# Kernel optimization log

Hardware: AMD Instinct MI355X
Metric: run time of the kernel (lower is better)

The kernel has to match this reference:

```python
import jax, jax.numpy as jnp
import numpy as np

B = 131072
USER_N = 100000
ITEM_N = 20000
CONCEPT_N = 128
D_IN = 3
NB_MOD_MAX = 12
M = NB_MOD_MAX + 2  # nb_mod_max_plus_sent


def setup_inputs() -> dict:
    key = jax.random.key(0)
    ks = jax.random.split(key, 7)
    user_ids = jax.random.randint(ks[0], (B,), 0, USER_N)
    item_ids = jax.random.randint(ks[1], (B,), 0, ITEM_N)
    concept_ids = jax.random.randint(ks[2], (B,), 0, CONCEPT_N)
    users_emb_weight = jax.random.normal(ks[3], (USER_N, CONCEPT_N), dtype=jnp.float32)
    item_resp_weight = jax.random.normal(ks[4], (ITEM_N * M, D_IN), dtype=jnp.float32)
    W = jax.random.normal(ks[5], (CONCEPT_N, D_IN, CONCEPT_N), dtype=jnp.float32)
    # nb_modalities in [2, nb_mod_max]; mask[i, j] = 0 for j in [1, nb_modalities[i]], inf elsewhere
    nb_modalities = jax.random.randint(ks[6], (ITEM_N,), 2, NB_MOD_MAX + 1)
    cols = jnp.arange(M)[None, :]  # (1, M)
    valid = (cols >= 1) & (cols <= nb_modalities[:, None])
    mask = jnp.where(valid, 0.0, jnp.inf).astype(jnp.float32)  # (ITEM_N, M)
    return {
        "user_ids": user_ids,
        "item_ids": item_ids,
        "concept_ids": concept_ids,
        "users_emb_weight": users_emb_weight,
        "item_resp_weight": item_resp_weight,
        "W": W,
        "mask": mask,
        "nb_modalities": nb_modalities,
    }


def reference(user_ids, item_ids, concept_ids, users_emb_weight, item_resp_weight, W, mask, nb_modalities):
    # W_t: (B, d_in, C)
    W_t = W[concept_ids]
    # im_idx: (B, M) row indices into the item-response embedding table
    im_idx = item_ids[:, None] * M + jnp.arange(M)[None, :]
    im_emb_prime = item_resp_weight[im_idx]  # (B, M, d_in)
    # bmm: (B, M, d_in) x (B, d_in, C) -> (B, M, C)
    im_emb = jnp.einsum('bmd,bdc->bmc', im_emb_prime, W_t)
    u_emb = users_emb_weight[user_ids]  # (B, C)
    diff = u_emb[:, None, :] - im_emb
    p_uim = jnp.sum(diff * diff, axis=2)  # (B, M)
    idx = jnp.argmin(p_uim + mask[item_ids, :], axis=1)  # (B,)
    nb = nb_modalities[item_ids]
    # mod_to_resp: ((idx - 1) / (nb - 1)) + 1
    responses = (idx.astype(jnp.float32) - 1.0) / (nb.astype(jnp.float32) - 1.0) + 1.0
    return responses
```

## Files before the change

kernel.cpp:

```cpp
#include <hip/hip_runtime.h>
#include <math.h>

static constexpr int B_TOTAL   = 131072;
static constexpr int M_MOD     = 14;
static constexpr int C_DIM     = 128;
static constexpr int CONCEPT_N = 128;

__global__ __launch_bounds__(64) void gram_kernel(
    const float* __restrict__ W,
    float*       __restrict__ Gt)
{
    const int c = blockIdx.x;
    const int l = threadIdx.x;
    const float* wp = W + (size_t)c * 3 * C_DIM;
    float g00 = 0.f, g01 = 0.f, g02 = 0.f, g11 = 0.f, g12 = 0.f, g22 = 0.f;
#pragma unroll
    for (int k = 0; k < 2; ++k) {
        const int col = l + 64 * k;
        const float a0 = wp[col];
        const float a1 = wp[C_DIM + col];
        const float a2 = wp[2 * C_DIM + col];
        g00 = fmaf(a0, a0, g00); g01 = fmaf(a0, a1, g01);
        g02 = fmaf(a0, a2, g02); g11 = fmaf(a1, a1, g11);
        g12 = fmaf(a1, a2, g12); g22 = fmaf(a2, a2, g22);
    }
#pragma unroll
    for (int off = 32; off; off >>= 1) {
        g00 += __shfl_xor(g00, off, 64);
        g01 += __shfl_xor(g01, off, 64);
        g02 += __shfl_xor(g02, off, 64);
        g11 += __shfl_xor(g11, off, 64);
        g12 += __shfl_xor(g12, off, 64);
        g22 += __shfl_xor(g22, off, 64);
    }
    if (l == 0) {
        float* gp = Gt + (size_t)c * 8;
        gp[0] = g00; gp[1] = g01; gp[2] = g02; gp[3] = g11;
        gp[4] = g12; gp[5] = g22; gp[6] = 0.f; gp[7] = 0.f;
    }
}

template <bool PRECOMP_G>
__global__ __launch_bounds__(256) void impact_kernel(
    const int*   __restrict__ user_ids,
    const int*   __restrict__ item_ids,
    const int*   __restrict__ concept_ids,
    const float* __restrict__ users_emb,
    const float* __restrict__ item_resp,
    const float* __restrict__ W,
    const int*   __restrict__ nb_mod,
    const float* __restrict__ Gt,
    float*       __restrict__ out)
{
    const int s = threadIdx.x & 15;
    const int b = blockIdx.x * 16 + (threadIdx.x >> 4);

    const int uid = user_ids[b];
    const int iid = item_ids[b];
    const int cid = concept_ids[b];
    const int nb  = nb_mod[iid];

    const int jl = (s < 12) ? (s + 1) : 1;
    const float* pj = item_resp + ((size_t)iid * M_MOD + jl) * 3;
    const float p0 = pj[0], p1 = pj[1], p2 = pj[2];

    const float4* up = (const float4*)(users_emb + (size_t)uid * C_DIM);
    const float4 uA = up[s], uB = up[s + 16];
    const float4* wp = (const float4*)(W + (size_t)cid * 3 * C_DIM);
    const float4 w0a = wp[s],      w0b = wp[16 + s];
    const float4 w1a = wp[32 + s], w1b = wp[48 + s];
    const float4 w2a = wp[64 + s], w2b = wp[80 + s];

    float v0 = 0.f, v1 = 0.f, v2 = 0.f;
    float g00, g01, g02, g11, g12, g22;

    if (PRECOMP_G) {
        const float4* gp = (const float4*)(Gt + (size_t)cid * 8);
        const float4 gA = gp[0], gB = gp[1];
        g00 = gA.x; g01 = gA.y; g02 = gA.z; g11 = gA.w;
        g12 = gB.x; g22 = gB.y;
#define COLV(uc, a0, a1, a2)                                                   \
        do {                                                                   \
            v0 = fmaf((a0), (uc), v0);                                         \
            v1 = fmaf((a1), (uc), v1);                                         \
            v2 = fmaf((a2), (uc), v2);                                         \
        } while (0)
        COLV(uA.x, w0a.x, w1a.x, w2a.x);
        COLV(uA.y, w0a.y, w1a.y, w2a.y);
        COLV(uA.z, w0a.z, w1a.z, w2a.z);
        COLV(uA.w, w0a.w, w1a.w, w2a.w);
        COLV(uB.x, w0b.x, w1b.x, w2b.x);
        COLV(uB.y, w0b.y, w1b.y, w2b.y);
        COLV(uB.z, w0b.z, w1b.z, w2b.z);
        COLV(uB.w, w0b.w, w1b.w, w2b.w);
#undef COLV
#pragma unroll
        for (int off = 8; off; off >>= 1) {
            v0 += __shfl_xor(v0, off, 64);
            v1 += __shfl_xor(v1, off, 64);
            v2 += __shfl_xor(v2, off, 64);
        }
    } else {
        g00 = 0.f; g01 = 0.f; g02 = 0.f; g11 = 0.f; g12 = 0.f; g22 = 0.f;
#define COL(uc, a0, a1, a2)                                                    \
        do {                                                                   \
            v0  = fmaf((a0), (uc), v0);  v1  = fmaf((a1), (uc), v1);           \
            v2  = fmaf((a2), (uc), v2);                                        \
            g00 = fmaf((a0), (a0), g00); g01 = fmaf((a0), (a1), g01);          \
            g02 = fmaf((a0), (a2), g02); g11 = fmaf((a1), (a1), g11);          \
            g12 = fmaf((a1), (a2), g12); g22 = fmaf((a2), (a2), g22);          \
        } while (0)
        COL(uA.x, w0a.x, w1a.x, w2a.x);
        COL(uA.y, w0a.y, w1a.y, w2a.y);
        COL(uA.z, w0a.z, w1a.z, w2a.z);
        COL(uA.w, w0a.w, w1a.w, w2a.w);
        COL(uB.x, w0b.x, w1b.x, w2b.x);
        COL(uB.y, w0b.y, w1b.y, w2b.y);
        COL(uB.z, w0b.z, w1b.z, w2b.z);
        COL(uB.w, w0b.w, w1b.w, w2b.w);
#undef COL
#pragma unroll
        for (int off = 8; off; off >>= 1) {
            v0  += __shfl_xor(v0,  off, 64);
            v1  += __shfl_xor(v1,  off, 64);
            v2  += __shfl_xor(v2,  off, 64);
            g00 += __shfl_xor(g00, off, 64);
            g01 += __shfl_xor(g01, off, 64);
            g02 += __shfl_xor(g02, off, 64);
            g11 += __shfl_xor(g11, off, 64);
            g12 += __shfl_xor(g12, off, 64);
            g22 += __shfl_xor(g22, off, 64);
        }
    }

    float m = INFINITY;
    if (s < 12 && (s + 1) <= nb) {
        const float dot = fmaf(p0, v0, fmaf(p1, v1, p2 * v2));
        float q = p0 * p0 * g00;
        q = fmaf(p1 * p1, g11, q);
        q = fmaf(p2 * p2, g22, q);
        q = fmaf(2.0f * p0 * p1, g01, q);
        q = fmaf(2.0f * p0 * p2, g02, q);
        q = fmaf(2.0f * p1 * p2, g12, q);
        m = fmaf(-2.0f, dot, q);
    }
    float bm = m;
#pragma unroll
    for (int off = 8; off; off >>= 1)
        bm = fminf(bm, __shfl_xor(bm, off, 64));
    const unsigned long long mask = __ballot(m == bm);
    if (s == 0) {
        const int group = (threadIdx.x >> 4) & 3;
        const unsigned slice = (unsigned)((mask >> (group * 16)) & 0xffffu);
        const int jm1 = __builtin_ctz(slice);
        out[b] = (float)jm1 / (float)(nb - 1) + 1.0f;
    }
}

extern "C" void kernel_launch(void* const* d_in, const int* in_sizes, int n_in,
                              void* d_out, int out_size, void* d_ws, size_t ws_size,
                              hipStream_t stream) {
    const int*   user_ids    = (const int*)d_in[0];
    const int*   item_ids    = (const int*)d_in[1];
    const int*   concept_ids = (const int*)d_in[2];
    const float* users_emb   = (const float*)d_in[3];
    const float* item_resp   = (const float*)d_in[4];
    const float* W           = (const float*)d_in[5];
    const int*   nb_mod      = (const int*)d_in[7];
    float*       out         = (float*)d_out;

    const size_t gram_bytes = (size_t)CONCEPT_N * 8 * sizeof(float);

    dim3 grid(B_TOTAL / 16), block(256);
    if (d_ws != nullptr && ws_size >= gram_bytes) {
        float* Gt = (float*)d_ws;
        gram_kernel<<<dim3(CONCEPT_N), dim3(64), 0, stream>>>(W, Gt);
        impact_kernel<true><<<grid, block, 0, stream>>>(
            user_ids, item_ids, concept_ids, users_emb, item_resp, W, nb_mod,
            Gt, out);
    } else {
        impact_kernel<false><<<grid, block, 0, stream>>>(
            user_ids, item_ids, concept_ids, users_emb, item_resp, W, nb_mod,
            nullptr, out);
    }
}
```

Measured before the change: 113.7 us.

## Drop Gram precompute kernel and process two batch rows per 16-lane group

Removes the separate Gram-matrix kernel and computes the 3x3 Gram terms inline in the main kernel, so only one kernel is launched. Each 16-lane group now handles two batch rows, with all gathers for both rows issued up front to raise memory-level parallelism. The grid is halved and launch bounds request 4 blocks per CU. The cost is extra per-row FMAs and shuffles for the Gram terms plus higher register pressure from holding two rows of W and user embeddings.

```diff
diff --git a/kernel.cpp b/kernel.cpp
--- a/kernel.cpp
+++ b/kernel.cpp
@@ -1,47 +1,11 @@
 #include <hip/hip_runtime.h>
 #include <math.h>
 
-static constexpr int B_TOTAL   = 131072;
-static constexpr int M_MOD     = 14;
-static constexpr int C_DIM     = 128;
-static constexpr int CONCEPT_N = 128;
+static constexpr int B_TOTAL = 131072;
+static constexpr int M_MOD   = 14;
+static constexpr int C_DIM   = 128;
 
-__global__ __launch_bounds__(64) void gram_kernel(
-    const float* __restrict__ W,
-    float*       __restrict__ Gt)
-{
-    const int c = blockIdx.x;
-    const int l = threadIdx.x;
-    const float* wp = W + (size_t)c * 3 * C_DIM;
-    float g00 = 0.f, g01 = 0.f, g02 = 0.f, g11 = 0.f, g12 = 0.f, g22 = 0.f;
-#pragma unroll
-    for (int k = 0; k < 2; ++k) {
-        const int col = l + 64 * k;
-        const float a0 = wp[col];
-        const float a1 = wp[C_DIM + col];
-        const float a2 = wp[2 * C_DIM + col];
-        g00 = fmaf(a0, a0, g00); g01 = fmaf(a0, a1, g01);
-        g02 = fmaf(a0, a2, g02); g11 = fmaf(a1, a1, g11);
-        g12 = fmaf(a1, a2, g12); g22 = fmaf(a2, a2, g22);
-    }
-#pragma unroll
-    for (int off = 32; off; off >>= 1) {
-        g00 += __shfl_xor(g00, off, 64);
-        g01 += __shfl_xor(g01, off, 64);
-        g02 += __shfl_xor(g02, off, 64);
-        g11 += __shfl_xor(g11, off, 64);
-        g12 += __shfl_xor(g12, off, 64);
-        g22 += __shfl_xor(g22, off, 64);
-    }
-    if (l == 0) {
-        float* gp = Gt + (size_t)c * 8;
-        gp[0] = g00; gp[1] = g01; gp[2] = g02; gp[3] = g11;
-        gp[4] = g12; gp[5] = g22; gp[6] = 0.f; gp[7] = 0.f;
-    }
-}
-
-template <bool PRECOMP_G>
-__global__ __launch_bounds__(256) void impact_kernel(
+__global__ __launch_bounds__(256, 4) void impact_kernel(
     const int*   __restrict__ user_ids,
     const int*   __restrict__ item_ids,
     const int*   __restrict__ concept_ids,
@@ -49,112 +13,120 @@
     const float* __restrict__ item_resp,
     const float* __restrict__ W,
     const int*   __restrict__ nb_mod,
-    const float* __restrict__ Gt,
     float*       __restrict__ out)
 {
     const int s = threadIdx.x & 15;
-    const int b = blockIdx.x * 16 + (threadIdx.x >> 4);
+    const int g = threadIdx.x >> 4;
+    const int b0 = blockIdx.x * 32 + g * 2;
+    const int b1 = b0 + 1;
 
-    const int uid = user_ids[b];
-    const int iid = item_ids[b];
-    const int cid = concept_ids[b];
-    const int nb  = nb_mod[iid];
+    const int uid0 = user_ids[b0],    uid1 = user_ids[b1];
+    const int iid0 = item_ids[b0],    iid1 = item_ids[b1];
+    const int cid0 = concept_ids[b0], cid1 = concept_ids[b1];
+    const int nb0  = nb_mod[iid0],    nb1  = nb_mod[iid1];
 
     const int jl = (s < 12) ? (s + 1) : 1;
-    const float* pj = item_resp + ((size_t)iid * M_MOD + jl) * 3;
-    const float p0 = pj[0], p1 = pj[1], p2 = pj[2];
+    const float* pj0 = item_resp + ((size_t)iid0 * M_MOD + jl) * 3;
+    const float* pj1 = item_resp + ((size_t)iid1 * M_MOD + jl) * 3;
+    const float p00 = pj0[0], p01 = pj0[1], p02 = pj0[2];
+    const float p10 = pj1[0], p11 = pj1[1], p12 = pj1[2];
 
-    const float4* up = (const float4*)(users_emb + (size_t)uid * C_DIM);
-    const float4 uA = up[s], uB = up[s + 16];
-    const float4* wp = (const float4*)(W + (size_t)cid * 3 * C_DIM);
-    const float4 w0a = wp[s],      w0b = wp[16 + s];
-    const float4 w1a = wp[32 + s], w1b = wp[48 + s];
-    const float4 w2a = wp[64 + s], w2b = wp[80 + s];
+    const float4* up0 = (const float4*)(users_emb + (size_t)uid0 * C_DIM);
+    const float4* up1 = (const float4*)(users_emb + (size_t)uid1 * C_DIM);
+    const float4 u0A = up0[s], u0B = up0[s + 16];
+    const float4 u1A = up1[s], u1B = up1[s + 16];
 
-    float v0 = 0.f, v1 = 0.f, v2 = 0.f;
-    float g00, g01, g02, g11, g12, g22;
+    const float4* wp0 = (const float4*)(W + (size_t)cid0 * 3 * C_DIM);
+    const float4* wp1 = (const float4*)(W + (size_t)cid1 * 3 * C_DIM);
+    const float4 x0a = wp0[s],      x0b = wp0[16 + s];
+    const float4 x1a = wp0[32 + s], x1b = wp0[48 + s];
+    const float4 x2a = wp0[64 + s], x2b = wp0[80 + s];
+    const float4 y0a = wp1[s],      y0b = wp1[16 + s];
+    const float4 y1a = wp1[32 + s], y1b = wp1[48 + s];
+    const float4 y2a = wp1[64 + s], y2b = wp1[80 + s];
 
-    if (PRECOMP_G) {
-        const float4* gp = (const float4*)(Gt + (size_t)cid * 8);
-        const float4 gA = gp[0], gB = gp[1];
-        g00 = gA.x; g01 = gA.y; g02 = gA.z; g11 = gA.w;
-        g12 = gB.x; g22 = gB.y;
-#define COLV(uc, a0, a1, a2)                                                   \
-        do {                                                                   \
-            v0 = fmaf((a0), (uc), v0);                                         \
-            v1 = fmaf((a1), (uc), v1);                                         \
-            v2 = fmaf((a2), (uc), v2);                                         \
-        } while (0)
-        COLV(uA.x, w0a.x, w1a.x, w2a.x);
-        COLV(uA.y, w0a.y, w1a.y, w2a.y);
-        COLV(uA.z, w0a.z, w1a.z, w2a.z);
-        COLV(uA.w, w0a.w, w1a.w, w2a.w);
-        COLV(uB.x, w0b.x, w1b.x, w2b.x);
-        COLV(uB.y, w0b.y, w1b.y, w2b.y);
-        COLV(uB.z, w0b.z, w1b.z, w2b.z);
-        COLV(uB.w, w0b.w, w1b.w, w2b.w);
-#undef COLV
-#pragma unroll
-        for (int off = 8; off; off >>= 1) {
-            v0 += __shfl_xor(v0, off, 64);
-            v1 += __shfl_xor(v1, off, 64);
-            v2 += __shfl_xor(v2, off, 64);
-        }
-    } else {
-        g00 = 0.f; g01 = 0.f; g02 = 0.f; g11 = 0.f; g12 = 0.f; g22 = 0.f;
 #define COL(uc, a0, a1, a2)                                                    \
-        do {                                                                   \
-            v0  = fmaf((a0), (uc), v0);  v1  = fmaf((a1), (uc), v1);           \
-            v2  = fmaf((a2), (uc), v2);                                        \
-            g00 = fmaf((a0), (a0), g00); g01 = fmaf((a0), (a1), g01);          \
-            g02 = fmaf((a0), (a2), g02); g11 = fmaf((a1), (a1), g11);          \
-            g12 = fmaf((a1), (a2), g12); g22 = fmaf((a2), (a2), g22);          \
-        } while (0)
-        COL(uA.x, w0a.x, w1a.x, w2a.x);
-        COL(uA.y, w0a.y, w1a.y, w2a.y);
-        COL(uA.z, w0a.z, w1a.z, w2a.z);
-        COL(uA.w, w0a.w, w1a.w, w2a.w);
-        COL(uB.x, w0b.x, w1b.x, w2b.x);
-        COL(uB.y, w0b.y, w1b.y, w2b.y);
-        COL(uB.z, w0b.z, w1b.z, w2b.z);
-        COL(uB.w, w0b.w, w1b.w, w2b.w);
-#undef COL
-#pragma unroll
-        for (int off = 8; off; off >>= 1) {
-            v0  += __shfl_xor(v0,  off, 64);
-            v1  += __shfl_xor(v1,  off, 64);
-            v2  += __shfl_xor(v2,  off, 64);
-            g00 += __shfl_xor(g00, off, 64);
-            g01 += __shfl_xor(g01, off, 64);
-            g02 += __shfl_xor(g02, off, 64);
-            g11 += __shfl_xor(g11, off, 64);
-            g12 += __shfl_xor(g12, off, 64);
-            g22 += __shfl_xor(g22, off, 64);
-        }
+    do {                                                                       \
+        v0  = fmaf((a0), (uc), v0);  v1  = fmaf((a1), (uc), v1);               \
+        v2  = fmaf((a2), (uc), v2);                                            \
+        g00 = fmaf((a0), (a0), g00); g01 = fmaf((a0), (a1), g01);              \
+        g02 = fmaf((a0), (a2), g02); g11 = fmaf((a1), (a1), g11);              \
+        g12 = fmaf((a1), (a2), g12); g22 = fmaf((a2), (a2), g22);              \
+    } while (0)
+
+#define REDUCE9()                                                              \
+    _Pragma("unroll")                                                          \
+    for (int off = 8; off; off >>= 1) {                                        \
+        v0  += __shfl_xor(v0,  off, 64);                                       \
+        v1  += __shfl_xor(v1,  off, 64);                                       \
+        v2  += __shfl_xor(v2,  off, 64);                                       \
+        g00 += __shfl_xor(g00, off, 64);                                       \
+        g01 += __shfl_xor(g01, off, 64);                                       \
+        g02 += __shfl_xor(g02, off, 64);                                       \
+        g11 += __shfl_xor(g11, off, 64);                                       \
+        g12 += __shfl_xor(g12, off, 64);                                       \
+        g22 += __shfl_xor(g22, off, 64);                                       \
     }
 
-    float m = INFINITY;
-    if (s < 12 && (s + 1) <= nb) {
-        const float dot = fmaf(p0, v0, fmaf(p1, v1, p2 * v2));
-        float q = p0 * p0 * g00;
-        q = fmaf(p1 * p1, g11, q);
-        q = fmaf(p2 * p2, g22, q);
-        q = fmaf(2.0f * p0 * p1, g01, q);
-        q = fmaf(2.0f * p0 * p2, g02, q);
-        q = fmaf(2.0f * p1 * p2, g12, q);
-        m = fmaf(-2.0f, dot, q);
+#define SCORE_AND_WRITE(P0, P1, P2, NB, BIDX)                                  \
+    do {                                                                       \
+        float m = INFINITY;                                                    \
+        if (s < 12 && (s + 1) <= (NB)) {                                       \
+            const float dot = fmaf((P0), v0, fmaf((P1), v1, (P2) * v2));       \
+            float q = (P0) * (P0) * g00;                                       \
+            q = fmaf((P1) * (P1), g11, q);                                     \
+            q = fmaf((P2) * (P2), g22, q);                                     \
+            q = fmaf(2.0f * (P0) * (P1), g01, q);                              \
+            q = fmaf(2.0f * (P0) * (P2), g02, q);                              \
+            q = fmaf(2.0f * (P1) * (P2), g12, q);                              \
+            m = fmaf(-2.0f, dot, q);                                           \
+        }                                                                      \
+        float bm = m;                                                          \
+        _Pragma("unroll")                                                      \
+        for (int off = 8; off; off >>= 1)                                      \
+            bm = fminf(bm, __shfl_xor(bm, off, 64));                           \
+        const unsigned long long mask = __ballot(m == bm);                     \
+        if (s == 0) {                                                          \
+            const int grp = g & 3;                                             \
+            const unsigned slice = (unsigned)((mask >> (grp * 16)) & 0xffffu); \
+            const int jm1 = __builtin_ctz(slice);                              \
+            out[BIDX] = (float)jm1 / (float)((NB) - 1) + 1.0f;                 \
+        }                                                                      \
+    } while (0)
+
+    {
+        float v0 = 0.f, v1 = 0.f, v2 = 0.f;
+        float g00 = 0.f, g01 = 0.f, g02 = 0.f, g11 = 0.f, g12 = 0.f, g22 = 0.f;
+        COL(u0A.x, x0a.x, x1a.x, x2a.x);
+        COL(u0A.y, x0a.y, x1a.y, x2a.y);
+        COL(u0A.z, x0a.z, x1a.z, x2a.z);
+        COL(u0A.w, x0a.w, x1a.w, x2a.w);
+        COL(u0B.x, x0b.x, x1b.x, x2b.x);
+        COL(u0B.y, x0b.y, x1b.y, x2b.y);
+        COL(u0B.z, x0b.z, x1b.z, x2b.z);
+        COL(u0B.w, x0b.w, x1b.w, x2b.w);
+        REDUCE9();
+        SCORE_AND_WRITE(p00, p01, p02, nb0, b0);
     }
-    float bm = m;
-#pragma unroll
-    for (int off = 8; off; off >>= 1)
-        bm = fminf(bm, __shfl_xor(bm, off, 64));
-    const unsigned long long mask = __ballot(m == bm);
-    if (s == 0) {
-        const int group = (threadIdx.x >> 4) & 3;
-        const unsigned slice = (unsigned)((mask >> (group * 16)) & 0xffffu);
-        const int jm1 = __builtin_ctz(slice);
-        out[b] = (float)jm1 / (float)(nb - 1) + 1.0f;
+
+    {
+        float v0 = 0.f, v1 = 0.f, v2 = 0.f;
+        float g00 = 0.f, g01 = 0.f, g02 = 0.f, g11 = 0.f, g12 = 0.f, g22 = 0.f;
+        COL(u1A.x, y0a.x, y1a.x, y2a.x);
+        COL(u1A.y, y0a.y, y1a.y, y2a.y);
+        COL(u1A.z, y0a.z, y1a.z, y2a.z);
+        COL(u1A.w, y0a.w, y1a.w, y2a.w);
+        COL(u1B.x, y0b.x, y1b.x, y2b.x);
+        COL(u1B.y, y0b.y, y1b.y, y2b.y);
+        COL(u1B.z, y0b.z, y1b.z, y2b.z);
+        COL(u1B.w, y0b.w, y1b.w, y2b.w);
+        REDUCE9();
+        SCORE_AND_WRITE(p10, p11, p12, nb1, b1);
     }
+
+#undef COL
+#undef REDUCE9
+#undef SCORE_AND_WRITE
 }
 
 extern "C" void kernel_launch(void* const* d_in, const int* in_sizes, int n_in,
@@ -169,18 +141,7 @@
     const int*   nb_mod      = (const int*)d_in[7];
     float*       out         = (float*)d_out;
 
-    const size_t gram_bytes = (size_t)CONCEPT_N * 8 * sizeof(float);
-
-    dim3 grid(B_TOTAL / 16), block(256);
-    if (d_ws != nullptr && ws_size >= gram_bytes) {
-        float* Gt = (float*)d_ws;
-        gram_kernel<<<dim3(CONCEPT_N), dim3(64), 0, stream>>>(W, Gt);
-        impact_kernel<true><<<grid, block, 0, stream>>>(
-            user_ids, item_ids, concept_ids, users_emb, item_resp, W, nb_mod,
-            Gt, out);
-    } else {
-        impact_kernel<false><<<grid, block, 0, stream>>>(
-            user_ids, item_ids, concept_ids, users_emb, item_resp, W, nb_mod,
-            nullptr, out);
-    }
+    dim3 grid(B_TOTAL / 32), block(256);
+    impact_kernel<<<grid, block, 0, stream>>>(user_ids, item_ids, concept_ids,
+                                              users_emb, item_resp, W, nb_mod, out);
 }
```

New measurement: 113.1 us. No clear change (-0.6%).

## Bin batch elements by user id to improve embedding gather locality

Applied to the files above, without the earlier changes.

Adds a zero kernel and an atomic scatter kernel that bucket batch indices into 1024 bins by user-id range, then processes elements bin by bin so nearby user embedding rows are read together. The precomputed per-concept Gram matrix is dropped and recomputed inline. This adds two extra launches, atomics, a workspace round trip and many early-exit blocks in exchange for better cache locality on the user table.

```diff
diff --git a/kernel.cpp b/kernel.cpp
--- a/kernel.cpp
+++ b/kernel.cpp
@@ -1,136 +1,124 @@
 #include <hip/hip_runtime.h>
 #include <math.h>
-
-static constexpr int B_TOTAL   = 131072;
-static constexpr int M_MOD     = 14;
-static constexpr int C_DIM     = 128;
-static constexpr int CONCEPT_N = 128;
-
-__global__ __launch_bounds__(64) void gram_kernel(
-    const float* __restrict__ W,
-    float*       __restrict__ Gt)
+#include <stdint.h>
+
+static constexpr int B_TOTAL = 131072;
+static constexpr int M_MOD   = 14;
+static constexpr int C_DIM   = 128;
+
+static constexpr int NBINS    = 1024;
+static constexpr int BIN_CAP  = 256;
+static constexpr int NSLOTS   = NBINS * BIN_CAP;
+static constexpr int BIN_BLKS = NSLOTS / 16;
+static constexpr int OVF_BLKS = B_TOTAL / 16;
+
+static constexpr size_t WS_SLOTS_OFF = 8192;
+static constexpr size_t WS_OVF_OFF   = WS_SLOTS_OFF + (size_t)NSLOTS * 8;
+static constexpr size_t WS_NEEDED    = WS_OVF_OFF + (size_t)B_TOTAL * 8;
+
+__global__ __launch_bounds__(1024) void zero_kernel(uint32_t* __restrict__ cnt) {
+    const int i = threadIdx.x;
+    cnt[i] = 0u;
+    if (i == 0) cnt[NBINS] = 0u;
+}
+
+__global__ __launch_bounds__(256) void scatter_kernel(
+    const int* __restrict__ user_ids,
+    uint32_t*  __restrict__ cnt,
+    uint64_t*  __restrict__ slots,
+    uint64_t*  __restrict__ ovf)
 {
-    const int c = blockIdx.x;
-    const int l = threadIdx.x;
-    const float* wp = W + (size_t)c * 3 * C_DIM;
+    const int e   = blockIdx.x * 256 + threadIdx.x;
+    const int uid = user_ids[e];
+    const int bin = uid >> 7;
+    const uint64_t pk = ((uint64_t)(uint32_t)uid << 32) | (uint32_t)e;
+    const uint32_t r = atomicAdd(&cnt[bin], 1u);
+    if (r < (uint32_t)BIN_CAP) {
+        slots[(size_t)bin * BIN_CAP + r] = pk;
+    } else {
+        const uint32_t o = atomicAdd(&cnt[NBINS], 1u);
+        ovf[o] = pk;
+    }
+}
+
+__global__ __launch_bounds__(256) void impact_binned(
+    const int*      __restrict__ item_ids,
+    const int*      __restrict__ concept_ids,
+    const float*    __restrict__ users_emb,
+    const float*    __restrict__ item_resp,
+    const float*    __restrict__ W,
+    const int*      __restrict__ nb_mod,
+    const uint32_t* __restrict__ cnt,
+    const uint64_t* __restrict__ slots,
+    const uint64_t* __restrict__ ovf,
+    float*          __restrict__ out)
+{
+    const int s = threadIdx.x & 15;
+    const int g = threadIdx.x >> 4;
+
+    uint64_t pk;
+    if (blockIdx.x < BIN_BLKS) {
+        const int bin  = blockIdx.x >> 4;
+        const int base = (blockIdx.x & 15) * 16;
+        uint32_t n = cnt[bin];
+        if (n > (uint32_t)BIN_CAP) n = BIN_CAP;
+        if ((uint32_t)(base + g) >= n) return;
+        pk = slots[(size_t)bin * BIN_CAP + base + g];
+    } else {
+        const uint32_t base = (uint32_t)(blockIdx.x - BIN_BLKS) * 16u;
+        const uint32_t n = cnt[NBINS];
+        if (base + (uint32_t)g >= n) return;
+        pk = ovf[base + g];
+    }
+
+    const int e   = (int)(uint32_t)pk;
+    const int uid = (int)(uint32_t)(pk >> 32);
+    const int iid = item_ids[e];
+    const int cid = concept_ids[e];
+    const int nb  = nb_mod[iid];
+
+    const int jl = (s < 12) ? (s + 1) : 1;
+    const float* pj = item_resp + ((size_t)iid * M_MOD + jl) * 3;
+    const float p0 = pj[0], p1 = pj[1], p2 = pj[2];
+
+    const float4* up = (const float4*)(users_emb + (size_t)uid * C_DIM);
+    const float4 uA = up[s], uB = up[s + 16];
+    const float4* wp = (const float4*)(W + (size_t)cid * 3 * C_DIM);
+    const float4 w0a = wp[s],      w0b = wp[16 + s];
+    const float4 w1a = wp[32 + s], w1b = wp[48 + s];
+    const float4 w2a = wp[64 + s], w2b = wp[80 + s];
+
+    float v0 = 0.f, v1 = 0.f, v2 = 0.f;
     float g00 = 0.f, g01 = 0.f, g02 = 0.f, g11 = 0.f, g12 = 0.f, g22 = 0.f;
-#pragma unroll
-    for (int k = 0; k < 2; ++k) {
-        const int col = l + 64 * k;
-        const float a0 = wp[col];
-        const float a1 = wp[C_DIM + col];
-        const float a2 = wp[2 * C_DIM + col];
-        g00 = fmaf(a0, a0, g00); g01 = fmaf(a0, a1, g01);
-        g02 = fmaf(a0, a2, g02); g11 = fmaf(a1, a1, g11);
-        g12 = fmaf(a1, a2, g12); g22 = fmaf(a2, a2, g22);
-    }
-#pragma unroll
-    for (int off = 32; off; off >>= 1) {
+#define COL(uc, a0, a1, a2)                                                    \
+    do {                                                                       \
+        v0  = fmaf((a0), (uc), v0);  v1  = fmaf((a1), (uc), v1);               \
+        v2  = fmaf((a2), (uc), v2);                                            \
+        g00 = fmaf((a0), (a0), g00); g01 = fmaf((a0), (a1), g01);              \
+        g02 = fmaf((a0), (a2), g02); g11 = fmaf((a1), (a1), g11);              \
+        g12 = fmaf((a1), (a2), g12); g22 = fmaf((a2), (a2), g22);              \
+    } while (0)
+    COL(uA.x, w0a.x, w1a.x, w2a.x);
+    COL(uA.y, w0a.y, w1a.y, w2a.y);
+    COL(uA.z, w0a.z, w1a.z, w2a.z);
+    COL(uA.w, w0a.w, w1a.w, w2a.w);
+    COL(uB.x, w0b.x, w1b.x, w2b.x);
+    COL(uB.y, w0b.y, w1b.y, w2b.y);
+    COL(uB.z, w0b.z, w1b.z, w2b.z);
+    COL(uB.w, w0b.w, w1b.w, w2b.w);
+#undef COL
+
+#pragma unroll
+    for (int off = 8; off; off >>= 1) {
+        v0  += __shfl_xor(v0,  off, 64);
+        v1  += __shfl_xor(v1,  off, 64);
+        v2  += __shfl_xor(v2,  off, 64);
         g00 += __shfl_xor(g00, off, 64);
         g01 += __shfl_xor(g01, off, 64);
         g02 += __shfl_xor(g02, off, 64);
         g11 += __shfl_xor(g11, off, 64);
         g12 += __shfl_xor(g12, off, 64);
         g22 += __shfl_xor(g22, off, 64);
-    }
-    if (l == 0) {
-        float* gp = Gt + (size_t)c * 8;
-        gp[0] = g00; gp[1] = g01; gp[2] = g02; gp[3] = g11;
-        gp[4] = g12; gp[5] = g22; gp[6] = 0.f; gp[7] = 0.f;
-    }
-}
-
-template <bool PRECOMP_G>
-__global__ __launch_bounds__(256) void impact_kernel(
-    const int*   __restrict__ user_ids,
-    const int*   __restrict__ item_ids,
-    const int*   __restrict__ concept_ids,
-    const float* __restrict__ users_emb,
-    const float* __restrict__ item_resp,
-    const float* __restrict__ W,
-    const int*   __restrict__ nb_mod,
-    const float* __restrict__ Gt,
-    float*       __restrict__ out)
-{
-    const int s = threadIdx.x & 15;
-    const int b = blockIdx.x * 16 + (threadIdx.x >> 4);
-
-    const int uid = user_ids[b];
-    const int iid = item_ids[b];
-    const int cid = concept_ids[b];
-    const int nb  = nb_mod[iid];
-
-    const int jl = (s < 12) ? (s + 1) : 1;
-    const float* pj = item_resp + ((size_t)iid * M_MOD + jl) * 3;
-    const float p0 = pj[0], p1 = pj[1], p2 = pj[2];
-
-    const float4* up = (const float4*)(users_emb + (size_t)uid * C_DIM);
-    const float4 uA = up[s], uB = up[s + 16];
-    const float4* wp = (const float4*)(W + (size_t)cid * 3 * C_DIM);
-    const float4 w0a = wp[s],      w0b = wp[16 + s];
-    const float4 w1a = wp[32 + s], w1b = wp[48 + s];
-    const float4 w2a = wp[64 + s], w2b = wp[80 + s];
-
-    float v0 = 0.f, v1 = 0.f, v2 = 0.f;
-    float g00, g01, g02, g11, g12, g22;
-
-    if (PRECOMP_G) {
-        const float4* gp = (const float4*)(Gt + (size_t)cid * 8);
-        const float4 gA = gp[0], gB = gp[1];
-        g00 = gA.x; g01 = gA.y; g02 = gA.z; g11 = gA.w;
-        g12 = gB.x; g22 = gB.y;
-#define COLV(uc, a0, a1, a2)                                                   \
-        do {                                                                   \
-            v0 = fmaf((a0), (uc), v0);                                         \
-            v1 = fmaf((a1), (uc), v1);                                         \
-            v2 = fmaf((a2), (uc), v2);                                         \
-        } while (0)
-        COLV(uA.x, w0a.x, w1a.x, w2a.x);
-        COLV(uA.y, w0a.y, w1a.y, w2a.y);
-        COLV(uA.z, w0a.z, w1a.z, w2a.z);
-        COLV(uA.w, w0a.w, w1a.w, w2a.w);
-        COLV(uB.x, w0b.x, w1b.x, w2b.x);
-        COLV(uB.y, w0b.y, w1b.y, w2b.y);
-        COLV(uB.z, w0b.z, w1b.z, w2b.z);
-        COLV(uB.w, w0b.w, w1b.w, w2b.w);
-#undef COLV
-#pragma unroll
-        for (int off = 8; off; off >>= 1) {
-            v0 += __shfl_xor(v0, off, 64);
-            v1 += __shfl_xor(v1, off, 64);
-            v2 += __shfl_xor(v2, off, 64);
-        }
-    } else {
-        g00 = 0.f; g01 = 0.f; g02 = 0.f; g11 = 0.f; g12 = 0.f; g22 = 0.f;
-#define COL(uc, a0, a1, a2)                                                    \
-        do {                                                                   \
-            v0  = fmaf((a0), (uc), v0);  v1  = fmaf((a1), (uc), v1);           \
-            v2  = fmaf((a2), (uc), v2);                                        \
-            g00 = fmaf((a0), (a0), g00); g01 = fmaf((a0), (a1), g01);          \
-            g02 = fmaf((a0), (a2), g02); g11 = fmaf((a1), (a1), g11);          \
-            g12 = fmaf((a1), (a2), g12); g22 = fmaf((a2), (a2), g22);          \
-        } while (0)
-        COL(uA.x, w0a.x, w1a.x, w2a.x);
-        COL(uA.y, w0a.y, w1a.y, w2a.y);
-        COL(uA.z, w0a.z, w1a.z, w2a.z);
-        COL(uA.w, w0a.w, w1a.w, w2a.w);
-        COL(uB.x, w0b.x, w1b.x, w2b.x);
-        COL(uB.y, w0b.y, w1b.y, w2b.y);
-        COL(uB.z, w0b.z, w1b.z, w2b.z);
-        COL(uB.w, w0b.w, w1b.w, w2b.w);
-#undef COL
-#pragma unroll
-        for (int off = 8; off; off >>= 1) {
-            v0  += __shfl_xor(v0,  off, 64);
-            v1  += __shfl_xor(v1,  off, 64);
-            v2  += __shfl_xor(v2,  off, 64);
-            g00 += __shfl_xor(g00, off, 64);
-            g01 += __shfl_xor(g01, off, 64);
-            g02 += __shfl_xor(g02, off, 64);
-            g11 += __shfl_xor(g11, off, 64);
-            g12 += __shfl_xor(g12, off, 64);
-            g22 += __shfl_xor(g22, off, 64);
-        }
     }
 
     float m = INFINITY;
@@ -150,8 +138,92 @@
         bm = fminf(bm, __shfl_xor(bm, off, 64));
     const unsigned long long mask = __ballot(m == bm);
     if (s == 0) {
-        const int group = (threadIdx.x >> 4) & 3;
-        const unsigned slice = (unsigned)((mask >> (group * 16)) & 0xffffu);
+        const int grp = g & 3;
+        const unsigned slice = (unsigned)((mask >> (grp * 16)) & 0xffffu);
+        const int jm1 = __builtin_ctz(slice);
+        out[e] = (float)jm1 / (float)(nb - 1) + 1.0f;
+    }
+}
+
+__global__ __launch_bounds__(256) void impact_direct(
+    const int*   __restrict__ user_ids,
+    const int*   __restrict__ item_ids,
+    const int*   __restrict__ concept_ids,
+    const float* __restrict__ users_emb,
+    const float* __restrict__ item_resp,
+    const float* __restrict__ W,
+    const int*   __restrict__ nb_mod,
+    float*       __restrict__ out)
+{
+    const int s = threadIdx.x & 15;
+    const int b = blockIdx.x * 16 + (threadIdx.x >> 4);
+
+    const int uid = user_ids[b];
+    const int iid = item_ids[b];
+    const int cid = concept_ids[b];
+    const int nb  = nb_mod[iid];
+
+    const int jl = (s < 12) ? (s + 1) : 1;
+    const float* pj = item_resp + ((size_t)iid * M_MOD + jl) * 3;
+    const float p0 = pj[0], p1 = pj[1], p2 = pj[2];
+
+    const float4* up = (const float4*)(users_emb + (size_t)uid * C_DIM);
+    const float4 uA = up[s], uB = up[s + 16];
+    const float4* wp = (const float4*)(W + (size_t)cid * 3 * C_DIM);
+    const float4 w0a = wp[s],      w0b = wp[16 + s];
+    const float4 w1a = wp[32 + s], w1b = wp[48 + s];
+    const float4 w2a = wp[64 + s], w2b = wp[80 + s];
+
+    float v0 = 0.f, v1 = 0.f, v2 = 0.f;
+    float g00 = 0.f, g01 = 0.f, g02 = 0.f, g11 = 0.f, g12 = 0.f, g22 = 0.f;
+#define COL(uc, a0, a1, a2)                                                    \
+    do {                                                                       \
+        v0  = fmaf((a0), (uc), v0);  v1  = fmaf((a1), (uc), v1);               \
+        v2  = fmaf((a2), (uc), v2);                                            \
+        g00 = fmaf((a0), (a0), g00); g01 = fmaf((a0), (a1), g01);              \
+        g02 = fmaf((a0), (a2), g02); g11 = fmaf((a1), (a1), g11);              \
+        g12 = fmaf((a1), (a2), g12); g22 = fmaf((a2), (a2), g22);              \
+    } while (0)
+    COL(uA.x, w0a.x, w1a.x, w2a.x);
+    COL(uA.y, w0a.y, w1a.y, w2a.y);
+    COL(uA.z, w0a.z, w1a.z, w2a.z);
+    COL(uA.w, w0a.w, w1a.w, w2a.w);
+    COL(uB.x, w0b.x, w1b.x, w2b.x);
+    COL(uB.y, w0b.y, w1b.y, w2b.y);
+    COL(uB.z, w0b.z, w1b.z, w2b.z);
+    COL(uB.w, w0b.w, w1b.w, w2b.w);
+#undef COL
+#pragma unroll
+    for (int off = 8; off; off >>= 1) {
+        v0  += __shfl_xor(v0,  off, 64);
+        v1  += __shfl_xor(v1,  off, 64);
+        v2  += __shfl_xor(v2,  off, 64);
+        g00 += __shfl_xor(g00, off, 64);
+        g01 += __shfl_xor(g01, off, 64);
+        g02 += __shfl_xor(g02, off, 64);
+        g11 += __shfl_xor(g11, off, 64);
+        g12 += __shfl_xor(g12, off, 64);
+        g22 += __shfl_xor(g22, off, 64);
+    }
+    float m = INFINITY;
+    if (s < 12 && (s + 1) <= nb) {
+        const float dot = fmaf(p0, v0, fmaf(p1, v1, p2 * v2));
+        float q = p0 * p0 * g00;
+        q = fmaf(p1 * p1, g11, q);
+        q = fmaf(p2 * p2, g22, q);
+        q = fmaf(2.0f * p0 * p1, g01, q);
+        q = fmaf(2.0f * p0 * p2, g02, q);
+        q = fmaf(2.0f * p1 * p2, g12, q);
+        m = fmaf(-2.0f, dot, q);
+    }
+    float bm = m;
+#pragma unroll
+    for (int off = 8; off; off >>= 1)
+        bm = fminf(bm, __shfl_xor(bm, off, 64));
+    const unsigned long long mask = __ballot(m == bm);
+    if (s == 0) {
+        const int grp = (threadIdx.x >> 4) & 3;
+        const unsigned slice = (unsigned)((mask >> (grp * 16)) & 0xffffu);
         const int jm1 = __builtin_ctz(slice);
         out[b] = (float)jm1 / (float)(nb - 1) + 1.0f;
     }
@@ -169,18 +241,19 @@
     const int*   nb_mod      = (const int*)d_in[7];
     float*       out         = (float*)d_out;
 
-    const size_t gram_bytes = (size_t)CONCEPT_N * 8 * sizeof(float);
-
-    dim3 grid(B_TOTAL / 16), block(256);
-    if (d_ws != nullptr && ws_size >= gram_bytes) {
-        float* Gt = (float*)d_ws;
-        gram_kernel<<<dim3(CONCEPT_N), dim3(64), 0, stream>>>(W, Gt);
-        impact_kernel<true><<<grid, block, 0, stream>>>(
+    if (d_ws != nullptr && ws_size >= WS_NEEDED) {
+        uint32_t* cnt   = (uint32_t*)d_ws;
+        uint64_t* slots = (uint64_t*)((char*)d_ws + WS_SLOTS_OFF);
+        uint64_t* ovf   = (uint64_t*)((char*)d_ws + WS_OVF_OFF);
+        zero_kernel<<<dim3(1), dim3(1024), 0, stream>>>(cnt);
+        scatter_kernel<<<dim3(B_TOTAL / 256), dim3(256), 0, stream>>>(
+            user_ids, cnt, slots, ovf);
+        impact_binned<<<dim3(BIN_BLKS + OVF_BLKS), dim3(256), 0, stream>>>(
+            item_ids, concept_ids, users_emb, item_resp, W, nb_mod,
+            cnt, slots, ovf, out);
+    } else {
+        impact_direct<<<dim3(B_TOTAL / 16), dim3(256), 0, stream>>>(
             user_ids, item_ids, concept_ids, users_emb, item_resp, W, nb_mod,
-            Gt, out);
-    } else {
-        impact_kernel<false><<<grid, block, 0, stream>>>(
-            user_ids, item_ids, concept_ids, users_emb, item_resp, W, nb_mod,
-            nullptr, out);
-    }
-}
+            out);
+    }
+}
```

Result: slower. 154.2 us (+35.6%).
